# Optimization experiments

Measured on AMD Instinct MI355X. Metric: run time of the kernel, lower is better.

Reference implementation:

```python
import jax, jax.numpy as jnp
import numpy as np

B, T, H = 32, 4096, 128   # batch, seq len, feature dim (ctor L=128)
N = 128                    # S5 state size (S5(dim, dim))
DEPTH = 2                  # L_LT
D_OUT = 64                 # adaptive pool output length (ctor D)
LN_EPS = 1e-5


def setup_inputs() -> dict:
    key = jax.random.key(0)
    ks = iter(jax.random.split(key, 40))
    def nrm(shape, s):
        return (jax.random.normal(next(ks), shape, jnp.float32) * s).astype(jnp.float32)
    inp = {}
    inp['x'] = jax.random.normal(next(ks), (B, T, H), jnp.float32)
    # LayerNorm params (stacked over depth)
    inp['ln1_g'] = jnp.ones((DEPTH, H), jnp.float32)
    inp['ln1_b'] = jnp.zeros((DEPTH, H), jnp.float32)
    inp['ln2_g'] = jnp.ones((DEPTH, H), jnp.float32)
    inp['ln2_b'] = jnp.zeros((DEPTH, H), jnp.float32)
    # S5 params: diagonal complex Lambda, complex B/C, real D skip, per-state log step
    inp['Lam_re'] = -0.5 * jnp.ones((DEPTH, N), jnp.float32)
    inp['Lam_im'] = jnp.tile(jnp.pi * jnp.arange(N, dtype=jnp.float32), (DEPTH, 1))
    inp['B_re'] = nrm((DEPTH, N, H), 1.0 / np.sqrt(H))
    inp['B_im'] = nrm((DEPTH, N, H), 1.0 / np.sqrt(H))
    inp['C_re'] = nrm((DEPTH, H, N), 1.0 / np.sqrt(N))
    inp['C_im'] = nrm((DEPTH, H, N), 1.0 / np.sqrt(N))
    inp['D_skip'] = nrm((DEPTH, H), 1.0)
    inp['log_step'] = jax.random.uniform(next(ks), (DEPTH, N), jnp.float32,
                                         minval=np.log(1e-3), maxval=np.log(1e-1))
    # MLP params
    inp['W1'] = nrm((DEPTH, H, 2 * H), 1.0 / np.sqrt(H))
    inp['b1'] = jnp.zeros((DEPTH, 2 * H), jnp.float32)
    inp['W2'] = nrm((DEPTH, 2 * H, H), 1.0 / np.sqrt(2 * H))
    inp['b2'] = jnp.zeros((DEPTH, H), jnp.float32)
    # Conv1d params (out_ch, in_ch, k=5)
    cs = 1.0 / np.sqrt(H * 5)
    inp['conv1_w'] = nrm((H, H, 5), cs)
    inp['conv1_b'] = jnp.zeros((H,), jnp.float32)
    inp['conv2_w'] = nrm((H, H, 5), cs)
    inp['conv2_b'] = jnp.zeros((H,), jnp.float32)
    return inp


def _layer_norm(x, g, b):
    mu = jnp.mean(x, axis=-1, keepdims=True)
    var = jnp.mean(jnp.square(x - mu), axis=-1, keepdims=True)
    return (x - mu) * jax.lax.rsqrt(var + LN_EPS) * g + b


def _s5(u, lam_re, lam_im, b_re, b_im, c_re, c_im, d_skip, log_step):
    # u: [B, T, H] real. Diagonal S5 with ZOH discretization + parallel scan.
    lam = lam_re + 1j * lam_im                       # (N,) complex
    dt = jnp.exp(log_step)                           # (N,)
    lam_bar = jnp.exp(lam * dt)                      # (N,)
    Bc = b_re + 1j * b_im                            # (N, H)
    B_bar = ((lam_bar - 1.0) / lam)[:, None] * Bc    # (N, H)
    Bu = jnp.einsum('bth,nh->btn', u.astype(jnp.complex64), B_bar)  # [B,T,N]
    A = jnp.broadcast_to(lam_bar.astype(jnp.complex64), Bu.shape)
    def binop(e1, e2):
        a1, x1 = e1
        a2, x2 = e2
        return a1 * a2, a2 * x1 + x2
    _, xs = jax.lax.associative_scan(binop, (A, Bu), axis=1)        # [B,T,N]
    Cc = c_re + 1j * c_im                            # (H, N)
    y = 2.0 * jnp.real(jnp.einsum('btn,hn->bth', xs, Cc)) + u * d_skip
    return y


def _conv1d_s2(x, w, b):
    # x: [B, C, L]; stride 2, padding 2, kernel 5
    y = jax.lax.conv_general_dilated(x, w, window_strides=(2,), padding=[(2, 2)],
                                     dimension_numbers=('NCH', 'OIH', 'NCH'))
    return y + b[None, :, None]


def reference(x, ln1_g, ln1_b, ln2_g, ln2_b, Lam_re, Lam_im, B_re, B_im,
              C_re, C_im, D_skip, log_step, W1, b1, W2, b2,
              conv1_w, conv1_b, conv2_w, conv2_b):
    for i in range(DEPTH):
        # S5 sub-block
        res = x
        xn = _layer_norm(x, ln1_g[i], ln1_b[i])
        x = res + _s5(xn, Lam_re[i], Lam_im[i], B_re[i], B_im[i],
                      C_re[i], C_im[i], D_skip[i], log_step[i])
        # MLP sub-block (dropout = identity in eval)
        res = x
        xn = _layer_norm(x, ln2_g[i], ln2_b[i])
        h = jax.nn.gelu(jnp.einsum('bth,hf->btf', xn, W1[i]) + b1[i], approximate=False)
        x = res + jnp.einsum('btf,fh->bth', h, W2[i]) + b2[i]
    x = jnp.transpose(x, (0, 2, 1))                  # [B, H, T]
    x = jax.nn.relu(_conv1d_s2(x, conv1_w, conv1_b))  # [B, H, T/2]
    x = jax.nn.relu(_conv1d_s2(x, conv2_w, conv2_b))  # [B, H, T/4]
    Lin = x.shape[-1]
    # AdaptiveAvgPool1d(D_OUT): Lin divisible by D_OUT -> uniform windows
    x = x.reshape(x.shape[0], x.shape[1], D_OUT, Lin // D_OUT).mean(axis=-1)
    return x  # [B, H, D_OUT]
```

## Files before the change

kernel.cpp:

```cpp
#include <hip/hip_runtime.h>
#include <math.h>

#define BATCH 32
#define TSEQ  4096
#define HD    128
#define NST   128
#define BT    (BATCH*TSEQ)
#define LC    64
#define NCHK  (TSEQ/LC)

typedef unsigned short bf16;
typedef __attribute__((ext_vector_type(8))) short bf16x8;
typedef __attribute__((ext_vector_type(4))) float f32x4;

__device__ inline float bf2f(bf16 s) {
    union { unsigned int u; float f; } v; v.u = ((unsigned int)s) << 16; return v.f;
}
__device__ inline bf16 f2bf(float f) {
    union { float f; unsigned int u; } v; v.f = f;
    unsigned int u = v.u;
    unsigned int r = (u + 0x7fffu + ((u >> 16) & 1u)) >> 16;
    return (bf16)r;
}
__device__ inline unsigned int pkpair(float lo, float hi) {
    union { float f; unsigned int u; } a, b;
    a.f = lo; b.f = hi;
    return __builtin_amdgcn_perm(b.u + 0x8000u, a.u + 0x8000u, 0x07060302u);
}
__device__ inline bf16x8 pack8f(float4 f0, float4 f1) {
    union { bf16x8 v; unsigned int u[4]; } t;
    t.u[0] = pkpair(f0.x, f0.y);
    t.u[1] = pkpair(f0.z, f0.w);
    t.u[2] = pkpair(f1.x, f1.y);
    t.u[3] = pkpair(f1.z, f1.w);
    return t.v;
}
__device__ inline float2 cmul2(float2 a, float2 b) {
    return make_float2(a.x*b.x - a.y*b.y, a.x*b.y + a.y*b.x);
}
__device__ inline float gelu_f(float x) {
    float u = x*(0.7978845608f + 0.0356774081f*x*x);
    return __fdividef(x, 1.f + __expf(-2.f*u));
}
__device__ inline float2 upk(unsigned int w) {
    union { unsigned int u; float f; } a, b;
    a.u = w << 16; b.u = w & 0xffff0000u;
    return make_float2(a.f, b.f);
}
__device__ inline unsigned int pk(float2 x) { return pkpair(x.x, x.y); }

__global__ void prep_s5(const float* __restrict__ Lam_re, const float* __restrict__ Lam_im,
                        const float* __restrict__ B_re,  const float* __restrict__ B_im,
                        const float* __restrict__ C_re,  const float* __restrict__ C_im,
                        const float* __restrict__ log_step,
                        const float* __restrict__ ln1_g, const float* __restrict__ ln1_b,
                        const float* __restrict__ D_skip,
                        bf16* __restrict__ Wbu_bf,
                        bf16* __restrict__ Wc_bf,
                        float* __restrict__ Sb, float* __restrict__ biasb,
                        float* __restrict__ gd, float* __restrict__ bd,
                        float4* __restrict__ coefs)
{
    int i = blockIdx.x, n = threadIdx.x;
    int in = i*NST + n;
    float lr = Lam_re[in], li = Lam_im[in];
    float dt = expf(log_step[in]);
    float ea = expf(lr*dt);
    float ar = ea*cosf(li*dt), ai = ea*sinf(li*dt);
    float xx = ar - 1.f, yy = ai;
    float den = lr*lr + li*li;
    float sr = (xx*lr + yy*li)/den;
    float si = (yy*lr - xx*li)/den;
    float2 p = make_float2(ar, ai);
    #pragma unroll
    for (int q = 0; q < 6; ++q) p = cmul2(p, p);
    coefs[in] = make_float4(ar, ai, p.x, p.y);

    const float* g  = ln1_g + i*HD;
    const float* bb = ln1_b + i*HD;
    const float* br = B_re + (size_t)in*HD;
    const float* bi = B_im + (size_t)in*HD;
    bf16* wb = Wbu_bf + (size_t)i*256*128;
    float s_re = 0.f, s_im = 0.f, bc_re = 0.f, bc_im = 0.f;
    for (int h = 0; h < HD; ++h) {
        float wre = sr*br[h] - si*bi[h];
        float wim = sr*bi[h] + si*br[h];
        bf16 wrb = f2bf(g[h]*wre), wib = f2bf(g[h]*wim);
        wb[(2*n)*128 + h]   = wrb;
        wb[(2*n+1)*128 + h] = wib;
        s_re += bf2f(wrb); s_im += bf2f(wib);
        bc_re += bb[h]*wre; bc_im += bb[h]*wim;
    }
    Sb[i*256 + 2*n] = s_re;     Sb[i*256 + 2*n+1] = s_im;
    biasb[i*256 + 2*n] = bc_re; biasb[i*256 + 2*n+1] = bc_im;

    const float* cr = C_re + (size_t)i*HD*NST;
    const float* ci = C_im + (size_t)i*HD*NST;
    bf16* wc = Wc_bf + (size_t)i*128*256;
    for (int h = 0; h < HD; ++h) {
        wc[h*256 + 2*n]   = f2bf( 2.f * cr[h*NST + n]);
        wc[h*256 + 2*n+1] = f2bf(-2.f * ci[h*NST + n]);
    }
    gd[i*HD + n] = g[n]*D_skip[i*HD + n];
    bd[i*HD + n] = bb[n]*D_skip[i*HD + n];
}

__global__ void prep_w1(const float* __restrict__ W1, const float* __restrict__ b1,
                        const float* __restrict__ ln2_g, const float* __restrict__ ln2_b,
                        bf16* __restrict__ W1_bf, float* __restrict__ S1,
                        float* __restrict__ bias1p)
{
    int i = blockIdx.x, f = threadIdx.x;
    const float* g  = ln2_g + i*HD;
    const float* bb = ln2_b + i*HD;
    bf16* w = W1_bf + (size_t)i*256*128;
    float S = 0.f, bi_ = b1[i*256 + f];
    for (int h = 0; h < HD; ++h) {
        float wv = W1[(size_t)i*32768 + h*256 + f];
        bf16 wbv = f2bf(g[h]*wv);
        w[f*128 + h] = wbv;
        S += bf2f(wbv);
        bi_ += bb[h]*wv;
    }
    S1[i*256 + f] = S;
    bias1p[i*256 + f] = bi_;
}

__global__ void prep_w2(const float* __restrict__ W2, bf16* __restrict__ W2_bf)
{
    int i = blockIdx.x, h = threadIdx.x;
    bf16* w = W2_bf + (size_t)i*128*256;
    for (int f = 0; f < 256; ++f)
        w[h*256 + f] = f2bf(W2[(size_t)i*32768 + f*128 + h]);
}

__global__ void prep_wB(const float* __restrict__ w1, const float* __restrict__ w2,
                        bf16* __restrict__ wB1, bf16* __restrict__ wB2)
{
    int idx = blockIdx.x*256 + threadIdx.x;
    if (idx >= 163840) return;
    const float* w = (idx < 81920) ? w1 : w2;
    bf16* wb       = (idx < 81920) ? wB1 : wB2;
    int r   = idx % 81920;
    int c   = r / 640;
    int tap = (r % 640) / 128;
    int ic  = r % 128;
    wb[r] = f2bf(w[(c*128 + ic)*5 + tap]);
}

template<int UD, typename TA>
__global__ __launch_bounds__(1024, 4) void lngemm(
    const TA* __restrict__ A,
    const bf16* __restrict__ Bt,
    const float* __restrict__ Svec, const float* __restrict__ bvec,
    bf16* __restrict__ outB,
    float2* __restrict__ munrs)
{
    __shared__ bf16 Bs[256*136];
    __shared__ float Sl[256], bl[256];

    int tid = threadIdx.x;
    #pragma unroll
    for (int it = 0; it < 4; ++it) {
        int f = it*1024 + tid;
        int n = f >> 4, kk = (f & 15)*8;
        *(bf16x8*)&Bs[n*136 + kk] = *(const bf16x8*)(Bt + n*128 + kk);
    }
    if (tid < 256) { Sl[tid] = Svec[tid]; bl[tid] = bvec[tid]; }
    __syncthreads();

    int wid = tid >> 6, lane = tid & 63;
    int quad = lane >> 4, cl = lane & 15;
    int s = blockIdx.x*16 + wid;
    size_t row = (size_t)s*16 + cl;

    bf16x8 af[4];
    float sm = 0.f, sq = 0.f;
    if constexpr (sizeof(TA) == 2) {
        const bf16* ar = (const bf16*)A + row*128;
        #pragma unroll
        for (int ks = 0; ks < 4; ++ks) {
            af[ks] = *(const bf16x8*)(ar + quad*8 + ks*32);
            union { bf16x8 v; unsigned int u[4]; } aa; aa.v = af[ks];
            #pragma unroll
            for (int jp = 0; jp < 4; ++jp) {
                float2 vv = upk(aa.u[jp]);
                sm += vv.x + vv.y;
                sq += vv.x*vv.x + vv.y*vv.y;
            }
        }
    } else {
        const float* ar = (const float*)A + row*128;
        #pragma unroll
        for (int ks = 0; ks < 4; ++ks) {
            float4 f0 = *(const float4*)(ar + quad*8 + ks*32);
            float4 f1 = *(const float4*)(ar + quad*8 + ks*32 + 4);
            sm += f0.x + f0.y + f0.z + f0.w + f1.x + f1.y + f1.z + f1.w;
            sq += f0.x*f0.x + f0.y*f0.y + f0.z*f0.z + f0.w*f0.w
                + f1.x*f1.x + f1.y*f1.y + f1.z*f1.z + f1.w*f1.w;
            af[ks] = pack8f(f0, f1);
        }
    }
    sm += __shfl_xor(sm, 16); sm += __shfl_xor(sm, 32);
    sq += __shfl_xor(sq, 16); sq += __shfl_xor(sq, 32);
    float mu = sm * (1.f/128.f);
    float rs = rsqrtf(sq*(1.f/128.f) - mu*mu + 1e-5f);
    float mr = mu*rs;

    if constexpr (UD) {
        if (quad == 0) munrs[row] = make_float2(mu, rs);
    }

    #pragma unroll
    for (int half = 0; half < 2; ++half) {
        f32x4 acc[8] = {};
        #pragma unroll
        for (int nt = 0; nt < 8; ++nt) {
            const bf16* wrp = &Bs[((half*8+nt)*16 + cl)*136 + quad*8];
            #pragma unroll
            for (int ks = 0; ks < 4; ++ks)
                acc[nt] = __builtin_amdgcn_mfma_f32_16x16x32_bf16(
                              *(const bf16x8*)(wrp + ks*32), af[ks], acc[nt], 0, 0, 0);
        }
        #pragma unroll
        for (int nt = 0; nt < 8; ++nt) {
            int n0 = (half*8+nt)*16 + quad*4;
            float4 S4 = *(const float4*)&Sl[n0];
            float4 b4 = *(const float4*)&bl[n0];
            float4 o;
            o.x = rs*acc[nt][0] - mr*S4.x + b4.x;
            o.y = rs*acc[nt][1] - mr*S4.y + b4.y;
            o.z = rs*acc[nt][2] - mr*S4.z + b4.z;
            o.w = rs*acc[nt][3] - mr*S4.w + b4.w;
            if constexpr (!UD) {
                o.x = gelu_f(o.x); o.y = gelu_f(o.y);
                o.z = gelu_f(o.z); o.w = gelu_f(o.w);
            }
            uint2 pu = make_uint2(pkpair(o.x, o.y), pkpair(o.z, o.w));
            *(uint2*)(outB + row*256 + n0) = pu;
        }
    }
}

template<int EPI, typename TR>
__global__ __launch_bounds__(1024, 4) void gemm2(
    const bf16* __restrict__ A,
    const bf16* __restrict__ Bt,
    bf16* out,
    const float* __restrict__ bias,
    const TR* resid,
    const float2* __restrict__ munrs,
    const float* __restrict__ gdp, const float* __restrict__ bdp)
{
    __shared__ bf16 Bs[128*264];
    __shared__ float gdl[128], bdl[128];

    int tid = threadIdx.x;
    #pragma unroll
    for (int it = 0; it < 4; ++it) {
        int f = it*1024 + tid;
        int n = f >> 5, kk = (f & 31)*8;
        *(bf16x8*)&Bs[n*264 + kk] = *(const bf16x8*)(Bt + n*256 + kk);
    }
    if constexpr (EPI == 3) {
        if (tid < 128) { gdl[tid] = gdp[tid]; bdl[tid] = bdp[tid]; }
    } else {
        if (tid < 128) { gdl[tid] = bias[tid]; }
    }
    __syncthreads();

    int wid = tid >> 6, lane = tid & 63;
    int quad = lane >> 4, cl = lane & 15;
    int s = blockIdx.x*16 + wid;
    size_t row = (size_t)s*16 + cl;

    float mu = 0.f, rs = 0.f;
    if constexpr (EPI == 3) { float2 m2 = munrs[row]; mu = m2.x; rs = m2.y; }

    bf16x8 af[8];
    #pragma unroll
    for (int ks = 0; ks < 8; ++ks)
        af[ks] = *(const bf16x8*)(A + row*256 + quad*8 + ks*32);

    f32x4 acc[8] = {};
    #pragma unroll
    for (int nt = 0; nt < 8; ++nt) {
        const bf16* wrp = &Bs[(nt*16 + cl)*264 + quad*8];
        #pragma unroll
        for (int ks = 0; ks < 8; ++ks)
            acc[nt] = __builtin_amdgcn_mfma_f32_16x16x32_bf16(
                          *(const bf16x8*)(wrp + ks*32), af[ks], acc[nt], 0, 0, 0);
    }

    #pragma unroll
    for (int nt = 0; nt < 8; ++nt) {
        int n0 = nt*16 + quad*4;
        size_t oidx = row*128 + n0;
        float4 rv;
        if constexpr (sizeof(TR) == 2) {
            ushort4 u4 = *(const ushort4*)((const bf16*)resid + oidx);
            rv = make_float4(bf2f(u4.x), bf2f(u4.y), bf2f(u4.z), bf2f(u4.w));
        } else {
            rv = *(const float4*)((const float*)resid + oidx);
        }
        float4 o;
        if constexpr (EPI == 2) {
            float4 bv = *(const float4*)&gdl[n0];
            o.x = acc[nt][0] + bv.x + rv.x; o.y = acc[nt][1] + bv.y + rv.y;
            o.z = acc[nt][2] + bv.z + rv.z; o.w = acc[nt][3] + bv.w + rv.w;
        } else {
            float4 g4 = *(const float4*)&gdl[n0];
            float4 b4 = *(const float4*)&bdl[n0];
            o.x = rv.x + acc[nt][0] + (rv.x - mu)*rs*g4.x + b4.x;
            o.y = rv.y + acc[nt][1] + (rv.y - mu)*rs*g4.y + b4.y;
            o.z = rv.z + acc[nt][2] + (rv.z - mu)*rs*g4.z + b4.z;
            o.w = rv.w + acc[nt][3] + (rv.w - mu)*rs*g4.w + b4.w;
        }
        uint2 pu = make_uint2(pkpair(o.x, o.y), pkpair(o.z, o.w));
        *(uint2*)(out + oidx) = pu;
    }
}

__global__ __launch_bounds__(256) void scan_local(unsigned int* __restrict__ xs,
                                                  const float4* __restrict__ coefs,
                                                  float2* __restrict__ carry)
{
    int flat = blockIdx.x*256 + threadIdx.x;
    int n = flat & 127;
    int b = (flat >> 7) & 31;
    int c = flat >> 12;
    float4 cf = coefs[n];
    float2 a = make_float2(cf.x, cf.y);
    unsigned int* base = xs + ((size_t)(b*TSEQ + c*LC))*NST + n;
    float2 x = make_float2(0.f, 0.f);
    for (int j = 0; j < LC; ++j) {
        float2 v = upk(base[(size_t)j*NST]);
        x = make_float2(a.x*x.x - a.y*x.y + v.x, a.x*x.y + a.y*x.x + v.y);
        base[(size_t)j*NST] = pk(x);
    }
    carry[c*(BATCH*NST) + b*NST + n] = x;
}

__global__ void scan_carry(float2* __restrict__ carry, const float4* __restrict__ coefs)
{
    int flat = blockIdx.x*256 + threadIdx.x;
    int n = flat & 127;
    float4 cf = coefs[n];
    float2 aL = make_float2(cf.z, cf.w);
    float2 x = make_float2(0.f, 0.f);
    for (int c = 0; c < NCHK; ++c) {
        float2* p = carry + c*(BATCH*NST) + flat;
        float2 v = *p;
        *p = x;
        x = make_float2(aL.x*x.x - aL.y*x.y + v.x, aL.x*x.y + aL.y*x.x + v.y);
    }
}

__global__ __launch_bounds__(256) void scan_fix(unsigned int* __restrict__ xs,
                                                const float4* __restrict__ coefs,
                                                const float2* __restrict__ carry)
{
    int flat = blockIdx.x*256 + threadIdx.x;
    int n = flat & 127;
    int b = (flat >> 7) & 31;
    int c = flat >> 12;
    if (c == 0) return;
    float2 cin = carry[c*(BATCH*NST) + b*NST + n];
    float4 cf = coefs[n];
    float2 a = make_float2(cf.x, cf.y);
    unsigned int* base = xs + ((size_t)(b*TSEQ + c*LC))*NST + n;
    float2 p = a;
    for (int j = 0; j < LC; ++j) {
        float2 add = cmul2(p, cin);
        float2 v = upk(base[(size_t)j*NST]);
        base[(size_t)j*NST] = pk(make_float2(v.x + add.x, v.y + add.y));
        p = cmul2(p, a);
    }
}

__global__ __launch_bounds__(256, 4) void conv1_mfma(
    const bf16* __restrict__ X,
    const bf16* __restrict__ wB,
    const float* __restrict__ bias,
    bf16* __restrict__ out,
    int Tin, int Lout)
{
    __shared__ bf16 As[128][72];
    __shared__ bf16 Bs[128][72];
    int tid  = threadIdx.x;
    int lane = tid & 63;
    int wave = tid >> 6;
    int wm = wave >> 1, wn = wave & 1;
    int quad = lane >> 4, cl = lane & 15;
    int row0 = blockIdx.x * 128;
    int b  = row0 / Lout;
    int l0 = row0 % Lout;
    const bf16* Xb = X + (size_t)b*Tin*128;

    f32x4 acc[4][4] = {};

    for (int k0 = 0; k0 < 640; k0 += 64) {
        int tap = k0 / 128;
        int icb = k0 % 128;
        #pragma unroll
        for (int it = 0; it < 4; ++it) {
            int idx = it*256 + tid;
            int r = idx >> 3, kof = (idx & 7) * 8;
            int t = 2*(l0 + r) - 2 + tap;
            bf16x8 z = {0,0,0,0,0,0,0,0};
            if (t >= 0 && t < Tin) z = *(const bf16x8*)(Xb + (size_t)t*128 + icb + kof);
            *(bf16x8*)&As[r][kof] = z;
        }
        #pragma unroll
        for (int it = 0; it < 4; ++it) {
            int idx = it*256 + tid;
            int n = idx >> 3, kof = (idx & 7) * 8;
            *(bf16x8*)&Bs[n][kof] = *(const bf16x8*)(wB + (size_t)n*640 + k0 + kof);
        }
        __syncthreads();
        #pragma unroll
        for (int kk = 0; kk < 64; kk += 32) {
            bf16x8 af[4], bfr[4];
            #pragma unroll
            for (int i = 0; i < 4; ++i)
                af[i] = *(const bf16x8*)&As[wm*64 + i*16 + cl][kk + quad*8];
            #pragma unroll
            for (int j = 0; j < 4; ++j)
                bfr[j] = *(const bf16x8*)&Bs[wn*64 + j*16 + cl][kk + quad*8];
            #pragma unroll
            for (int i = 0; i < 4; ++i)
                #pragma unroll
                for (int j = 0; j < 4; ++j)
                    acc[i][j] = __builtin_amdgcn_mfma_f32_16x16x32_bf16(
                                    bfr[j], af[i], acc[i][j], 0, 0, 0);
        }
        __syncthreads();
    }

    #pragma unroll
    for (int i = 0; i < 4; ++i) {
        int grow = row0 + wm*64 + i*16 + cl;
        #pragma unroll
        for (int j = 0; j < 4; ++j) {
            int gcol = wn*64 + j*16 + quad*4;
            float4 bv = *(const float4*)(bias + gcol);
            float4 t;
            t.x = fmaxf(acc[i][j][0] + bv.x, 0.f); t.y = fmaxf(acc[i][j][1] + bv.y, 0.f);
            t.z = fmaxf(acc[i][j][2] + bv.z, 0.f); t.w = fmaxf(acc[i][j][3] + bv.w, 0.f);
            uint2 pu = make_uint2(pkpair(t.x, t.y), pkpair(t.z, t.w));
            *(uint2*)(out + (size_t)grow*128 + gcol) = pu;
        }
    }
}

__global__ __launch_bounds__(256, 4) void conv2_pool(
    const bf16* __restrict__ X,
    const bf16* __restrict__ wB,
    const float* __restrict__ bias,
    float* __restrict__ outp,
    int Tin, int Lout)
{
    __shared__ bf16 As[128][72];
    __shared__ bf16 Bs[128][72];
    int tid  = threadIdx.x;
    int lane = tid & 63;
    int wave = tid >> 6;
    int wm = wave >> 1, wn = wave & 1;
    int quad = lane >> 4, cl = lane & 15;
    int row0 = blockIdx.x * 128;
    int b  = row0 / Lout;
    int l0 = row0 % Lout;
    int d0 = l0 / 16;
    const bf16* Xb = X + (size_t)b*Tin*128;

    f32x4 acc[4][4] = {};

    for (int k0 = 0; k0 < 640; k0 += 64) {
        int tap = k0 / 128;
        int icb = k0 % 128;
        #pragma unroll
        for (int it = 0; it < 4; ++it) {
            int idx = it*256 + tid;
            int r = idx >> 3, kof = (idx & 7) * 8;
            int t = 2*(l0 + r) - 2 + tap;
            bf16x8 z = {0,0,0,0,0,0,0,0};
            if (t >= 0 && t < Tin) z = *(const bf16x8*)(Xb + (size_t)t*128 + icb + kof);
            *(bf16x8*)&As[r][kof] = z;
        }
        #pragma unroll
        for (int it = 0; it < 4; ++it) {
            int idx = it*256 + tid;
            int n = idx >> 3, kof = (idx & 7) * 8;
            *(bf16x8*)&Bs[n][kof] = *(const bf16x8*)(wB + (size_t)n*640 + k0 + kof);
        }
        __syncthreads();
        #pragma unroll
        for (int kk = 0; kk < 64; kk += 32) {
            bf16x8 af[4], bfr[4];
            #pragma unroll
            for (int i = 0; i < 4; ++i)
                af[i] = *(const bf16x8*)&As[wm*64 + i*16 + cl][kk + quad*8];
            #pragma unroll
            for (int j = 0; j < 4; ++j)
                bfr[j] = *(const bf16x8*)&Bs[wn*64 + j*16 + cl][kk + quad*8];
            #pragma unroll
            for (int i = 0; i < 4; ++i)
                #pragma unroll
                for (int j = 0; j < 4; ++j)
                    acc[i][j] = __builtin_amdgcn_mfma_f32_16x16x32_bf16(
                                    bfr[j], af[i], acc[i][j], 0, 0, 0);
        }
        __syncthreads();
    }

    #pragma unroll
    for (int j = 0; j < 4; ++j) {
        int gcol = wn*64 + j*16 + quad*4;
        float4 bv = *(const float4*)(bias + gcol);
        #pragma unroll
        for (int i = 0; i < 4; ++i) {
            float4 sp;
            sp.x = fmaxf(acc[i][j][0] + bv.x, 0.f);
            sp.y = fmaxf(acc[i][j][1] + bv.y, 0.f);
            sp.z = fmaxf(acc[i][j][2] + bv.z, 0.f);
            sp.w = fmaxf(acc[i][j][3] + bv.w, 0.f);
            #pragma unroll
            for (int off = 1; off <= 8; off <<= 1) {
                sp.x += __shfl_xor(sp.x, off);
                sp.y += __shfl_xor(sp.y, off);
                sp.z += __shfl_xor(sp.z, off);
                sp.w += __shfl_xor(sp.w, off);
            }
            if (cl == 0) {
                int d = d0 + wm*4 + i;
                float* op = outp + (size_t)b*8192 + (size_t)gcol*64 + d;
                op[0]   = sp.x * (1.f/16.f);
                op[64]  = sp.y * (1.f/16.f);
                op[128] = sp.z * (1.f/16.f);
                op[192] = sp.w * (1.f/16.f);
            }
        }
    }
}

extern "C" void kernel_launch(void* const* d_in, const int* in_sizes, int n_in,
                              void* d_out, int out_size, void* d_ws, size_t ws_size,
                              hipStream_t stream)
{
    (void)in_sizes; (void)n_in; (void)out_size; (void)ws_size;
    const float* x_in    = (const float*)d_in[0];
    const float* ln1_g   = (const float*)d_in[1];
    const float* ln1_b   = (const float*)d_in[2];
    const float* ln2_g   = (const float*)d_in[3];
    const float* ln2_b   = (const float*)d_in[4];
    const float* Lam_re  = (const float*)d_in[5];
    const float* Lam_im  = (const float*)d_in[6];
    const float* B_re    = (const float*)d_in[7];
    const float* B_im    = (const float*)d_in[8];
    const float* C_re    = (const float*)d_in[9];
    const float* C_im    = (const float*)d_in[10];
    const float* D_skip  = (const float*)d_in[11];
    const float* log_step= (const float*)d_in[12];
    const float* W1      = (const float*)d_in[13];
    const float* b1      = (const float*)d_in[14];
    const float* W2      = (const float*)d_in[15];
    const float* b2      = (const float*)d_in[16];
    const float* conv1_w = (const float*)d_in[17];
    const float* conv1_b = (const float*)d_in[18];
    const float* conv2_w = (const float*)d_in[19];
    const float* conv2_b = (const float*)d_in[20];
    float* out = (float*)d_out;

    char* ws = (char*)d_ws;
    bf16*   Xbf    = (bf16*) (ws);
    bf16*   Cbuf   = (bf16*) (ws + (size_t)33554432);
    bf16*   Cv1    = (bf16*) (ws + (size_t)100663296);
    float2* munrs  = (float2*)(ws + (size_t)117440512);
    char*   wreg   = ws + (size_t)118489088;
    bf16*   Wbu_bf = (bf16*)(wreg);
    bf16*   Wc_bf  = (bf16*)(wreg + 131072);
    bf16*   W1_bf  = (bf16*)(wreg + 262144);
    bf16*   W2_bf  = (bf16*)(wreg + 393216);
    float*  Sb     = (float*)(wreg + 524288);
    float*  biasb  = (float*)(wreg + 526336);
    float*  S1     = (float*)(wreg + 528384);
    float*  bias1p = (float*)(wreg + 530432);
    float*  gd     = (float*)(wreg + 532480);
    float*  bd     = (float*)(wreg + 533504);
    float4* coefs  = (float4*)(wreg + 534528);
    bf16*   wB1    = (bf16*)(wreg + 538624);
    bf16*   wB2    = (bf16*)(wreg + 702464);
    float2* carry  = (float2*)(wreg + 866304);

    prep_s5<<<2, 128, 0, stream>>>(Lam_re, Lam_im, B_re, B_im, C_re, C_im, log_step,
                                   ln1_g, ln1_b, D_skip,
                                   Wbu_bf, Wc_bf, Sb, biasb, gd, bd, coefs);
    prep_w1<<<2, 256, 0, stream>>>(W1, b1, ln2_g, ln2_b, W1_bf, S1, bias1p);
    prep_w2<<<2, 128, 0, stream>>>(W2, W2_bf);
    prep_wB<<<640, 256, 0, stream>>>(conv1_w, conv2_w, wB1, wB2);

    for (int i = 0; i < 2; ++i) {
        if (i == 0)
            lngemm<1, float><<<512, 1024, 0, stream>>>(
                x_in, Wbu_bf, Sb, biasb, Cbuf, munrs);
        else
            lngemm<1, bf16><<<512, 1024, 0, stream>>>(
                Xbf, Wbu_bf + 32768, Sb + 256, biasb + 256, Cbuf, munrs);
        scan_local<<<1024, 256, 0, stream>>>((unsigned int*)Cbuf, coefs + i*NST, carry);
        scan_carry<<<16, 256, 0, stream>>>(carry, coefs + i*NST);
        scan_fix<<<1024, 256, 0, stream>>>((unsigned int*)Cbuf, coefs + i*NST, carry);
        if (i == 0)
            gemm2<3, float><<<512, 1024, 0, stream>>>(
                Cbuf, Wc_bf, Xbf, nullptr, x_in, munrs, gd, bd);
        else
            gemm2<3, bf16><<<512, 1024, 0, stream>>>(
                Cbuf, Wc_bf + 32768, Xbf, nullptr, Xbf, munrs, gd + 128, bd + 128);
        lngemm<0, bf16><<<512, 1024, 0, stream>>>(
            Xbf, W1_bf + (size_t)i*32768, S1 + i*256, bias1p + i*256, Cbuf, nullptr);
        gemm2<2, bf16><<<512, 1024, 0, stream>>>(
            Cbuf, W2_bf + (size_t)i*32768, Xbf, b2 + i*HD, Xbf,
            nullptr, nullptr, nullptr);
    }

    conv1_mfma<<<512, 256, 0, stream>>>(Xbf, wB1, conv1_b, Cv1, 4096, 2048);
    conv2_pool<<<256, 256, 0, stream>>>(Cv1, wB2, conv2_b, out, 2048, 1024);
}
```

Baseline: 596.5 us.

## Switch row GEMMs to 32x32x16 MFMA with weights read directly from global

The LN+GEMM and second GEMM kernels now give each wave 32 rows and use 32x32x16 bf16 MFMA instead of 16x16x32. The LDS staging of weights, scale and bias vectors is dropped, along with the block barrier, so weights are read straight from global or L2. Blocks shrink from 1024 to 256 threads. The aim is to remove per-block LDS fill and sync overhead and to use the larger MFMA shape. The cost is uncoalesced, repeated global weight reads that rely on cache hits.

```diff
diff --git a/kernel.cpp b/kernel.cpp
--- a/kernel.cpp
+++ b/kernel.cpp
@@ -12,6 +12,7 @@
 typedef unsigned short bf16;
 typedef __attribute__((ext_vector_type(8))) short bf16x8;
 typedef __attribute__((ext_vector_type(4))) float f32x4;
+typedef __attribute__((ext_vector_type(16))) float f32x16;
 
 __device__ inline float bf2f(bf16 s) {
     union { unsigned int u; float f; } v; v.u = ((unsigned int)s) << 16; return v.f;
@@ -149,39 +150,28 @@
 }
 
 template<int UD, typename TA>
-__global__ __launch_bounds__(1024, 4) void lngemm(
+__global__ __launch_bounds__(256, 4) void lngemm(
     const TA* __restrict__ A,
     const bf16* __restrict__ Bt,
     const float* __restrict__ Svec, const float* __restrict__ bvec,
     bf16* __restrict__ outB,
     float2* __restrict__ munrs)
 {
-    __shared__ bf16 Bs[256*136];
-    __shared__ float Sl[256], bl[256];
-
     int tid = threadIdx.x;
-    #pragma unroll
-    for (int it = 0; it < 4; ++it) {
-        int f = it*1024 + tid;
-        int n = f >> 4, kk = (f & 15)*8;
-        *(bf16x8*)&Bs[n*136 + kk] = *(const bf16x8*)(Bt + n*128 + kk);
-    }
-    if (tid < 256) { Sl[tid] = Svec[tid]; bl[tid] = bvec[tid]; }
-    __syncthreads();
-
-    int wid = tid >> 6, lane = tid & 63;
-    int quad = lane >> 4, cl = lane & 15;
-    int s = blockIdx.x*16 + wid;
-    size_t row = (size_t)s*16 + cl;
-
-    bf16x8 af[4];
+    int wave = tid >> 6, lane = tid & 63;
+    int tl = lane & 31;
+    int kh = lane >> 5;
+    int s = blockIdx.x*4 + wave;
+    size_t row = (size_t)s*32 + tl;
+
+    bf16x8 af[8];
     float sm = 0.f, sq = 0.f;
     if constexpr (sizeof(TA) == 2) {
-        const bf16* ar = (const bf16*)A + row*128;
-        #pragma unroll
-        for (int ks = 0; ks < 4; ++ks) {
-            af[ks] = *(const bf16x8*)(ar + quad*8 + ks*32);
-            union { bf16x8 v; unsigned int u[4]; } aa; aa.v = af[ks];
+        const bf16* ar = (const bf16*)A + row*128 + kh*8;
+        #pragma unroll
+        for (int kt = 0; kt < 8; ++kt) {
+            af[kt] = *(const bf16x8*)(ar + kt*16);
+            union { bf16x8 v; unsigned int u[4]; } aa; aa.v = af[kt];
             #pragma unroll
             for (int jp = 0; jp < 4; ++jp) {
                 float2 vv = upk(aa.u[jp]);
@@ -190,48 +180,45 @@
             }
         }
     } else {
-        const float* ar = (const float*)A + row*128;
-        #pragma unroll
-        for (int ks = 0; ks < 4; ++ks) {
-            float4 f0 = *(const float4*)(ar + quad*8 + ks*32);
-            float4 f1 = *(const float4*)(ar + quad*8 + ks*32 + 4);
+        const float* ar = (const float*)A + row*128 + kh*8;
+        #pragma unroll
+        for (int kt = 0; kt < 8; ++kt) {
+            float4 f0 = *(const float4*)(ar + kt*16);
+            float4 f1 = *(const float4*)(ar + kt*16 + 4);
             sm += f0.x + f0.y + f0.z + f0.w + f1.x + f1.y + f1.z + f1.w;
             sq += f0.x*f0.x + f0.y*f0.y + f0.z*f0.z + f0.w*f0.w
                 + f1.x*f1.x + f1.y*f1.y + f1.z*f1.z + f1.w*f1.w;
-            af[ks] = pack8f(f0, f1);
-        }
-    }
-    sm += __shfl_xor(sm, 16); sm += __shfl_xor(sm, 32);
-    sq += __shfl_xor(sq, 16); sq += __shfl_xor(sq, 32);
+            af[kt] = pack8f(f0, f1);
+        }
+    }
+    sm += __shfl_xor(sm, 32);
+    sq += __shfl_xor(sq, 32);
     float mu = sm * (1.f/128.f);
     float rs = rsqrtf(sq*(1.f/128.f) - mu*mu + 1e-5f);
     float mr = mu*rs;
 
     if constexpr (UD) {
-        if (quad == 0) munrs[row] = make_float2(mu, rs);
+        if (kh == 0) munrs[row] = make_float2(mu, rs);
     }
 
     #pragma unroll
-    for (int half = 0; half < 2; ++half) {
-        f32x4 acc[8] = {};
-        #pragma unroll
-        for (int nt = 0; nt < 8; ++nt) {
-            const bf16* wrp = &Bs[((half*8+nt)*16 + cl)*136 + quad*8];
-            #pragma unroll
-            for (int ks = 0; ks < 4; ++ks)
-                acc[nt] = __builtin_amdgcn_mfma_f32_16x16x32_bf16(
-                              *(const bf16x8*)(wrp + ks*32), af[ks], acc[nt], 0, 0, 0);
-        }
-        #pragma unroll
-        for (int nt = 0; nt < 8; ++nt) {
-            int n0 = (half*8+nt)*16 + quad*4;
-            float4 S4 = *(const float4*)&Sl[n0];
-            float4 b4 = *(const float4*)&bl[n0];
+    for (int nt = 0; nt < 8; ++nt) {
+        const bf16* wr = Bt + (size_t)(nt*32 + tl)*128 + kh*8;
+        f32x16 acc = {};
+        #pragma unroll
+        for (int kt = 0; kt < 8; ++kt)
+            acc = __builtin_amdgcn_mfma_f32_32x32x16_bf16(
+                      *(const bf16x8*)(wr + kt*16), af[kt], acc, 0, 0, 0);
+        #pragma unroll
+        for (int rg = 0; rg < 4; ++rg) {
+            int n0 = nt*32 + rg*8 + kh*4;
+            float4 S4 = *(const float4*)&Svec[n0];
+            float4 b4 = *(const float4*)&bvec[n0];
             float4 o;
-            o.x = rs*acc[nt][0] - mr*S4.x + b4.x;
-            o.y = rs*acc[nt][1] - mr*S4.y + b4.y;
-            o.z = rs*acc[nt][2] - mr*S4.z + b4.z;
-            o.w = rs*acc[nt][3] - mr*S4.w + b4.w;
+            o.x = rs*acc[rg*4+0] - mr*S4.x + b4.x;
+            o.y = rs*acc[rg*4+1] - mr*S4.y + b4.y;
+            o.z = rs*acc[rg*4+2] - mr*S4.z + b4.z;
+            o.w = rs*acc[rg*4+3] - mr*S4.w + b4.w;
             if constexpr (!UD) {
                 o.x = gelu_f(o.x); o.y = gelu_f(o.y);
                 o.z = gelu_f(o.z); o.w = gelu_f(o.w);
@@ -243,7 +230,7 @@
 }
 
 template<int EPI, typename TR>
-__global__ __launch_bounds__(1024, 4) void gemm2(
+__global__ __launch_bounds__(256, 4) void gemm2(
     const bf16* __restrict__ A,
     const bf16* __restrict__ Bt,
     bf16* out,
@@ -252,72 +239,57 @@
     const float2* __restrict__ munrs,
     const float* __restrict__ gdp, const float* __restrict__ bdp)
 {
-    __shared__ bf16 Bs[128*264];
-    __shared__ float gdl[128], bdl[128];
-
     int tid = threadIdx.x;
-    #pragma unroll
-    for (int it = 0; it < 4; ++it) {
-        int f = it*1024 + tid;
-        int n = f >> 5, kk = (f & 31)*8;
-        *(bf16x8*)&Bs[n*264 + kk] = *(const bf16x8*)(Bt + n*256 + kk);
-    }
-    if constexpr (EPI == 3) {
-        if (tid < 128) { gdl[tid] = gdp[tid]; bdl[tid] = bdp[tid]; }
-    } else {
-        if (tid < 128) { gdl[tid] = bias[tid]; }
-    }
-    __syncthreads();
-
-    int wid = tid >> 6, lane = tid & 63;
-    int quad = lane >> 4, cl = lane & 15;
-    int s = blockIdx.x*16 + wid;
-    size_t row = (size_t)s*16 + cl;
+    int wave = tid >> 6, lane = tid & 63;
+    int tl = lane & 31;
+    int kh = lane >> 5;
+    int s = blockIdx.x*4 + wave;
+    size_t row = (size_t)s*32 + tl;
 
     float mu = 0.f, rs = 0.f;
     if constexpr (EPI == 3) { float2 m2 = munrs[row]; mu = m2.x; rs = m2.y; }
 
-    bf16x8 af[8];
+    bf16x8 af[16];
+    const bf16* ar = A + row*256 + kh*8;
     #pragma unroll
-    for (int ks = 0; ks < 8; ++ks)
-        af[ks] = *(const bf16x8*)(A + row*256 + quad*8 + ks*32);
-
-    f32x4 acc[8] = {};
+    for (int kt = 0; kt < 16; ++kt)
+        af[kt] = *(const bf16x8*)(ar + kt*16);
+
     #pragma unroll
-    for (int nt = 0; nt < 8; ++nt) {
-        const bf16* wrp = &Bs[(nt*16 + cl)*264 + quad*8];
-        #pragma unroll
-        for (int ks = 0; ks < 8; ++ks)
-            acc[nt] = __builtin_amdgcn_mfma_f32_16x16x32_bf16(
-                          *(const bf16x8*)(wrp + ks*32), af[ks], acc[nt], 0, 0, 0);
-    }
-
-    #pragma unroll
-    for (int nt = 0; nt < 8; ++nt) {
-        int n0 = nt*16 + quad*4;
-        size_t oidx = row*128 + n0;
-        float4 rv;
-        if constexpr (sizeof(TR) == 2) {
-            ushort4 u4 = *(const ushort4*)((const bf16*)resid + oidx);
-            rv = make_float4(bf2f(u4.x), bf2f(u4.y), bf2f(u4.z), bf2f(u4.w));
-        } else {
-            rv = *(const float4*)((const float*)resid + oidx);
-        }
-        float4 o;
-        if constexpr (EPI == 2) {
-            float4 bv = *(const float4*)&gdl[n0];
-            o.x = acc[nt][0] + bv.x + rv.x; o.y = acc[nt][1] + bv.y + rv.y;
-            o.z = acc[nt][2] + bv.z + rv.z; o.w = acc[nt][3] + bv.w + rv.w;
-        } else {
-            float4 g4 = *(const float4*)&gdl[n0];
-            float4 b4 = *(const float4*)&bdl[n0];
-            o.x = rv.x + acc[nt][0] + (rv.x - mu)*rs*g4.x + b4.x;
-            o.y = rv.y + acc[nt][1] + (rv.y - mu)*rs*g4.y + b4.y;
-            o.z = rv.z + acc[nt][2] + (rv.z - mu)*rs*g4.z + b4.z;
-            o.w = rv.w + acc[nt][3] + (rv.w - mu)*rs*g4.w + b4.w;
-        }
-        uint2 pu = make_uint2(pkpair(o.x, o.y), pkpair(o.z, o.w));
-        *(uint2*)(out + oidx) = pu;
+    for (int nt = 0; nt < 4; ++nt) {
+        const bf16* wr = Bt + (size_t)(nt*32 + tl)*256 + kh*8;
+        f32x16 acc = {};
+        #pragma unroll
+        for (int kt = 0; kt < 16; ++kt)
+            acc = __builtin_amdgcn_mfma_f32_32x32x16_bf16(
+                      *(const bf16x8*)(wr + kt*16), af[kt], acc, 0, 0, 0);
+        #pragma unroll
+        for (int rg = 0; rg < 4; ++rg) {
+            int n0 = nt*32 + rg*8 + kh*4;
+            size_t oidx = row*128 + n0;
+            float4 rv;
+            if constexpr (sizeof(TR) == 2) {
+                ushort4 u4 = *(const ushort4*)((const bf16*)resid + oidx);
+                rv = make_float4(bf2f(u4.x), bf2f(u4.y), bf2f(u4.z), bf2f(u4.w));
+            } else {
+                rv = *(const float4*)((const float*)resid + oidx);
+            }
+            float4 o;
+            if constexpr (EPI == 2) {
+                float4 bv = *(const float4*)&bias[n0];
+                o.x = acc[rg*4+0] + bv.x + rv.x; o.y = acc[rg*4+1] + bv.y + rv.y;
+                o.z = acc[rg*4+2] + bv.z + rv.z; o.w = acc[rg*4+3] + bv.w + rv.w;
+            } else {
+                float4 g4 = *(const float4*)&gdp[n0];
+                float4 b4 = *(const float4*)&bdp[n0];
+                o.x = rv.x + acc[rg*4+0] + (rv.x - mu)*rs*g4.x + b4.x;
+                o.y = rv.y + acc[rg*4+1] + (rv.y - mu)*rs*g4.y + b4.y;
+                o.z = rv.z + acc[rg*4+2] + (rv.z - mu)*rs*g4.z + b4.z;
+                o.w = rv.w + acc[rg*4+3] + (rv.w - mu)*rs*g4.w + b4.w;
+            }
+            uint2 pu = make_uint2(pkpair(o.x, o.y), pkpair(o.z, o.w));
+            *(uint2*)(out + oidx) = pu;
+        }
     }
 }
 
@@ -601,23 +573,23 @@
 
     for (int i = 0; i < 2; ++i) {
         if (i == 0)
-            lngemm<1, float><<<512, 1024, 0, stream>>>(
+            lngemm<1, float><<<1024, 256, 0, stream>>>(
                 x_in, Wbu_bf, Sb, biasb, Cbuf, munrs);
         else
-            lngemm<1, bf16><<<512, 1024, 0, stream>>>(
+            lngemm<1, bf16><<<1024, 256, 0, stream>>>(
                 Xbf, Wbu_bf + 32768, Sb + 256, biasb + 256, Cbuf, munrs);
         scan_local<<<1024, 256, 0, stream>>>((unsigned int*)Cbuf, coefs + i*NST, carry);
         scan_carry<<<16, 256, 0, stream>>>(carry, coefs + i*NST);
         scan_fix<<<1024, 256, 0, stream>>>((unsigned int*)Cbuf, coefs + i*NST, carry);
         if (i == 0)
-            gemm2<3, float><<<512, 1024, 0, stream>>>(
+            gemm2<3, float><<<1024, 256, 0, stream>>>(
                 Cbuf, Wc_bf, Xbf, nullptr, x_in, munrs, gd, bd);
         else
-            gemm2<3, bf16><<<512, 1024, 0, stream>>>(
+            gemm2<3, bf16><<<1024, 256, 0, stream>>>(
                 Cbuf, Wc_bf + 32768, Xbf, nullptr, Xbf, munrs, gd + 128, bd + 128);
-        lngemm<0, bf16><<<512, 1024, 0, stream>>>(
+        lngemm<0, bf16><<<1024, 256, 0, stream>>>(
             Xbf, W1_bf + (size_t)i*32768, S1 + i*256, bias1p + i*256, Cbuf, nullptr);
-        gemm2<2, bf16><<<512, 1024, 0, stream>>>(
+        gemm2<2, bf16><<<1024, 256, 0, stream>>>(
             Cbuf, W2_bf + (size_t)i*32768, Xbf, b2 + i*HD, Xbf,
             nullptr, nullptr, nullptr);
     }
```

New measurement: 782.9 us. 1.31x slower.

## Fuse scan carry fix-up into the output GEMM A-operand load

Applied to the files above, without the earlier changes.

Removes the scan_fix kernel, which re-read and rewrote the whole state buffer, and applies the chunk-carry correction inside gemm2 while loading A fragments. Powers of the diagonal transition are precomputed per step offset in prep_s5 and stored in a small table. This saves a full read-modify-write pass of the large state tensor per layer, at the cost of extra small loads and complex multiplies in the GEMM prologue.

```diff
diff --git a/kernel.cpp b/kernel.cpp
--- a/kernel.cpp
+++ b/kernel.cpp
@@ -59,7 +59,8 @@
                         bf16* __restrict__ Wc_bf,
                         float* __restrict__ Sb, float* __restrict__ biasb,
                         float* __restrict__ gd, float* __restrict__ bd,
-                        float4* __restrict__ coefs)
+                        float4* __restrict__ coefs,
+                        float2* __restrict__ apow)
 {
     int i = blockIdx.x, n = threadIdx.x;
     int in = i*NST + n;
@@ -71,10 +72,17 @@
     float den = lr*lr + li*li;
     float sr = (xx*lr + yy*li)/den;
     float si = (yy*lr - xx*li)/den;
-    float2 p = make_float2(ar, ai);
-    #pragma unroll
-    for (int q = 0; q < 6; ++q) p = cmul2(p, p);
-    coefs[in] = make_float4(ar, ai, p.x, p.y);
+    float2 a2 = make_float2(ar, ai);
+    float2 p = a2;
+    float2* apr = apow + (size_t)i*64*128;
+    for (int j = 0; j < 64; ++j) {
+        apr[j*128 + n] = p;
+        p = cmul2(p, a2);
+    }
+    float2 q = a2;
+    #pragma unroll
+    for (int t = 0; t < 6; ++t) q = cmul2(q, q);
+    coefs[in] = make_float4(ar, ai, q.x, q.y);
 
     const float* g  = ln1_g + i*HD;
     const float* bb = ln1_b + i*HD;
@@ -250,7 +258,9 @@
     const float* __restrict__ bias,
     const TR* resid,
     const float2* __restrict__ munrs,
-    const float* __restrict__ gdp, const float* __restrict__ bdp)
+    const float* __restrict__ gdp, const float* __restrict__ bdp,
+    const float2* __restrict__ carry,
+    const float2* __restrict__ apow)
 {
     __shared__ bf16 Bs[128*264];
     __shared__ float gdl[128], bdl[128];
@@ -278,9 +288,31 @@
     if constexpr (EPI == 3) { float2 m2 = munrs[row]; mu = m2.x; rs = m2.y; }
 
     bf16x8 af[8];
-    #pragma unroll
-    for (int ks = 0; ks < 8; ++ks)
-        af[ks] = *(const bf16x8*)(A + row*256 + quad*8 + ks*32);
+    const bf16* ar = A + row*256 + quad*8;
+    if constexpr (EPI == 3) {
+        int b  = (int)(row >> 12);
+        int tp = (int)(row & 4095);
+        int cc = tp >> 6, j = tp & 63;
+        const float2* cin = carry + (size_t)cc*(BATCH*NST) + (size_t)b*NST;
+        const float2* ap  = apow + (size_t)j*128;
+        #pragma unroll
+        for (int ks = 0; ks < 8; ++ks) {
+            union { bf16x8 v; unsigned int u[4]; } t;
+            t.v = *(const bf16x8*)(ar + ks*32);
+            int n0 = quad*4 + ks*16;
+            #pragma unroll
+            for (int jp = 0; jp < 4; ++jp) {
+                float2 v  = upk(t.u[jp]);
+                float2 ad = cmul2(ap[n0+jp], cin[n0+jp]);
+                t.u[jp] = pk(make_float2(v.x + ad.x, v.y + ad.y));
+            }
+            af[ks] = t.v;
+        }
+    } else {
+        #pragma unroll
+        for (int ks = 0; ks < 8; ++ks)
+            af[ks] = *(const bf16x8*)(ar + ks*32);
+    }
 
     f32x4 acc[8] = {};
     #pragma unroll
@@ -353,28 +385,6 @@
         float2 v = *p;
         *p = x;
         x = make_float2(aL.x*x.x - aL.y*x.y + v.x, aL.x*x.y + aL.y*x.x + v.y);
-    }
-}
-
-__global__ __launch_bounds__(256) void scan_fix(unsigned int* __restrict__ xs,
-                                                const float4* __restrict__ coefs,
-                                                const float2* __restrict__ carry)
-{
-    int flat = blockIdx.x*256 + threadIdx.x;
-    int n = flat & 127;
-    int b = (flat >> 7) & 31;
-    int c = flat >> 12;
-    if (c == 0) return;
-    float2 cin = carry[c*(BATCH*NST) + b*NST + n];
-    float4 cf = coefs[n];
-    float2 a = make_float2(cf.x, cf.y);
-    unsigned int* base = xs + ((size_t)(b*TSEQ + c*LC))*NST + n;
-    float2 p = a;
-    for (int j = 0; j < LC; ++j) {
-        float2 add = cmul2(p, cin);
-        float2 v = upk(base[(size_t)j*NST]);
-        base[(size_t)j*NST] = pk(make_float2(v.x + add.x, v.y + add.y));
-        p = cmul2(p, a);
     }
 }
 
@@ -591,10 +601,11 @@
     bf16*   wB1    = (bf16*)(wreg + 538624);
     bf16*   wB2    = (bf16*)(wreg + 702464);
     float2* carry  = (float2*)(wreg + 866304);
+    float2* apow   = (float2*)(wreg + 2963456);
 
     prep_s5<<<2, 128, 0, stream>>>(Lam_re, Lam_im, B_re, B_im, C_re, C_im, log_step,
                                    ln1_g, ln1_b, D_skip,
-                                   Wbu_bf, Wc_bf, Sb, biasb, gd, bd, coefs);
+                                   Wbu_bf, Wc_bf, Sb, biasb, gd, bd, coefs, apow);
     prep_w1<<<2, 256, 0, stream>>>(W1, b1, ln2_g, ln2_b, W1_bf, S1, bias1p);
     prep_w2<<<2, 128, 0, stream>>>(W2, W2_bf);
     prep_wB<<<640, 256, 0, stream>>>(conv1_w, conv2_w, wB1, wB2);
@@ -608,18 +619,19 @@
                 Xbf, Wbu_bf + 32768, Sb + 256, biasb + 256, Cbuf, munrs);
         scan_local<<<1024, 256, 0, stream>>>((unsigned int*)Cbuf, coefs + i*NST, carry);
         scan_carry<<<16, 256, 0, stream>>>(carry, coefs + i*NST);
-        scan_fix<<<1024, 256, 0, stream>>>((unsigned int*)Cbuf, coefs + i*NST, carry);
         if (i == 0)
             gemm2<3, float><<<512, 1024, 0, stream>>>(
-                Cbuf, Wc_bf, Xbf, nullptr, x_in, munrs, gd, bd);
+                Cbuf, Wc_bf, Xbf, nullptr, x_in, munrs, gd, bd,
+                carry, apow);
         else
             gemm2<3, bf16><<<512, 1024, 0, stream>>>(
-                Cbuf, Wc_bf + 32768, Xbf, nullptr, Xbf, munrs, gd + 128, bd + 128);
+                Cbuf, Wc_bf + 32768, Xbf, nullptr, Xbf, munrs, gd + 128, bd + 128,
+                carry, apow + 64*128);
         lngemm<0, bf16><<<512, 1024, 0, stream>>>(
             Xbf, W1_bf + (size_t)i*32768, S1 + i*256, bias1p + i*256, Cbuf, nullptr);
         gemm2<2, bf16><<<512, 1024, 0, stream>>>(
             Cbuf, W2_bf + (size_t)i*32768, Xbf, b2 + i*HD, Xbf,
-            nullptr, nullptr, nullptr);
+            nullptr, nullptr, nullptr, nullptr, nullptr);
     }
 
     conv1_mfma<<<512, 256, 0, stream>>>(Xbf, wB1, conv1_b, Cv1, 4096, 2048);
```

Result: faster. 569.4 us (median of 2 runs) (-4.5%).
